# Performance work log

Hardware: AMD Instinct MI355X
Metric: run time of the kernel (lower is better)

Reference implementation:

```python
import jax, jax.numpy as jnp
import numpy as np

B, N = 128, 128
FEAT_IN = 6   # feature_dim(4) + class + score
E = 32        # embedding_dim
NUM_CLASSES = 80


def setup_inputs() -> dict:
    key = jax.random.key(0)
    ks = jax.random.split(key, 20)
    def glorot(k, shape):
        fan_in, fan_out = shape[0], shape[1]
        lim = jnp.sqrt(6.0 / (fan_in + fan_out)).astype(jnp.float32)
        return jax.random.uniform(k, shape, jnp.float32, -lim, lim)
    return {
        'boxes': jax.random.uniform(ks[0], (B, N, 4), jnp.float32),
        'classes': jax.random.randint(ks[1], (B, N), 0, NUM_CLASSES),
        'scores': jax.random.uniform(ks[2], (B, N), jnp.float32),
        'num_objects': jax.random.randint(ks[3], (B,), 1, N + 1),
        # feature_encoder: Linear(6->32), ReLU, Linear(32->32)
        'W1': glorot(ks[4], (FEAT_IN, E)), 'b1': jnp.zeros((E,), jnp.float32),
        'W2': glorot(ks[5], (E, E)),       'b2': jnp.zeros((E,), jnp.float32),
        # isObject: Linear(32->32), ReLU, Linear(32->1), Sigmoid
        'Wo1': glorot(ks[6], (E, E)),  'bo1': jnp.zeros((E,), jnp.float32),
        'Wo2': glorot(ks[7], (E, 1)),  'bo2': jnp.zeros((1,), jnp.float32),
        # sameClass: Linear(64->32), ReLU, Linear(32->1), Sigmoid
        'Ws1': glorot(ks[8], (2 * E, E)), 'bs1': jnp.zeros((E,), jnp.float32),
        'Ws2': glorot(ks[9], (E, 1)),     'bs2': jnp.zeros((1,), jnp.float32),
    }


def reference(boxes, classes, scores, num_objects, W1, b1, W2, b2,
              Wo1, bo1, Wo2, bo2, Ws1, bs1, Ws2, bs2):
    # encode: [B,N,6] -> [B,N,E]
    combined = jnp.concatenate(
        [boxes, classes.astype(jnp.float32)[..., None], scores[..., None]], axis=-1)
    enc = jax.nn.relu(combined @ W1 + b1) @ W2 + b2                 # [B,N,E]

    # isObject predicate -> [B,N]
    isobj = jax.nn.sigmoid(jax.nn.relu(enc @ Wo1 + bo1) @ Wo2 + bo2)[..., 0]

    # sameClass on all pairs: split concat-weight so we never build [B,N,N,2E]
    Wsx, Wsy = Ws1[:E], Ws1[E:]
    hx = enc @ Wsx                                                  # [B,N,E]
    hy = enc @ Wsy                                                  # [B,N,E]
    h = jax.nn.relu(hx[:, :, None, :] + hy[:, None, :, :] + bs1)    # [B,N,N,E]
    same = jax.nn.sigmoid(h @ Ws2 + bs2)[..., 0]                    # [B,N,N] (x,y)

    # inner = And_min(isObject(y), sameClass(x,y))
    inner = jnp.minimum(isobj[:, None, :], same)                    # [B,N,N]

    mask = jnp.arange(N)[None, :] < num_objects[:, None]            # [B,N] valid objs
    n = num_objects.astype(jnp.float32)
    denom = jnp.maximum(n, 1.0)

    # Exists_y = mean over valid y
    exists = jnp.sum(inner * mask[:, None, :], axis=-1) / denom[:, None]  # [B,N]

    # outer = Or_max(Not(isObject(x)), exists)
    outer = jnp.maximum(1.0 - isobj, exists)                        # [B,N]

    # Forall_x = min over valid x (pad with 1.0, never the min for valid batches)
    sat_b = jnp.min(jnp.where(mask, outer, 1.0), axis=-1)           # [B]

    valid = (num_objects > 0).astype(jnp.float32)
    cnt = jnp.sum(valid)
    total = jnp.where(cnt > 0,
                      jnp.sum(sat_b * valid) / jnp.maximum(cnt, 1.0),
                      jnp.float32(1.0))
    return total
```

## Files before the change

### kernel.cpp

```cpp
#include <hip/hip_runtime.h>

#define BB 128
#define NN 128
#define EE 32

#define SAT_OFF 0
#define CNT_OFF 128
#define HX_OFF  256
#define HY_OFF  (HX_OFF + 16384 * 32)
#define ISO_OFF (HY_OFF + 16384 * 32)

__global__ __launch_bounds__(256) void encode_kernel(
    const float* __restrict__ boxes, const int* __restrict__ classes,
    const float* __restrict__ scores,
    const float* __restrict__ W1, const float* __restrict__ b1,
    const float* __restrict__ W2, const float* __restrict__ b2,
    const float* __restrict__ Wo1, const float* __restrict__ bo1,
    const float* __restrict__ Wo2, const float* __restrict__ bo2,
    const float* __restrict__ Ws1, float* __restrict__ ws)
{
    __shared__ float rows[8 * 36];

    const int t = threadIdx.x;
    const int e = t & 31;
    const int g = t >> 5;

    if (blockIdx.x == 0) {
        if (t < 128) ((unsigned*)ws)[SAT_OFF + t] = 0x7F7F7F7Fu;
        if (t == 128) ((unsigned*)ws)[CNT_OFF] = 0u;
    }

    float w1c[6];
#pragma unroll
    for (int f = 0; f < 6; f++) w1c[f] = W1[f * 32 + e];
    float w2c[32], wo1c[32], wsxc[32], wsyc[32];
#pragma unroll
    for (int k = 0; k < 32; k++) {
        w2c[k]  = W2[k * 32 + e];
        wo1c[k] = Wo1[k * 32 + e];
        wsxc[k] = Ws1[k * 32 + e];
        wsyc[k] = Ws1[(32 + k) * 32 + e];
    }
    const float b1e  = b1[e];
    const float b2e  = b2[e];
    const float bo1e = bo1[e];
    const float wo2e = Wo2[e];
    const float bo2s = bo2[0];

    float* row = rows + g * 36;
    const int itemBase = blockIdx.x * 32 + g * 4;

#pragma unroll 1
    for (int it = 0; it < 4; ++it) {
        const int item = itemBase + it;

        const float4 bx = ((const float4*)boxes)[item];
        const float c4 = (float)classes[item];
        const float c5 = scores[item];

        float h1 = b1e;
        h1 = fmaf(bx.x, w1c[0], h1);
        h1 = fmaf(bx.y, w1c[1], h1);
        h1 = fmaf(bx.z, w1c[2], h1);
        h1 = fmaf(bx.w, w1c[3], h1);
        h1 = fmaf(c4,   w1c[4], h1);
        h1 = fmaf(c5,   w1c[5], h1);
        h1 = fmaxf(h1, 0.f);

        row[e] = h1;

        float a0 = 0.f, a1 = 0.f, a2 = 0.f, a3 = 0.f;
#pragma unroll
        for (int kk = 0; kk < 8; kk++) {
            const float4 h = *(const float4*)(row + kk * 4);
            a0 = fmaf(h.x, w2c[4 * kk + 0], a0);
            a1 = fmaf(h.y, w2c[4 * kk + 1], a1);
            a2 = fmaf(h.z, w2c[4 * kk + 2], a2);
            a3 = fmaf(h.w, w2c[4 * kk + 3], a3);
        }
        const float enc = ((a0 + a1) + (a2 + a3)) + b2e;
        row[e] = enc;

        float u = bo1e, hx = 0.f, hy = 0.f;
#pragma unroll
        for (int kk = 0; kk < 8; kk++) {
            const float4 ec = *(const float4*)(row + kk * 4);
            const int k0 = 4 * kk;
            u  = fmaf(ec.x, wo1c[k0 + 0], u);
            u  = fmaf(ec.y, wo1c[k0 + 1], u);
            u  = fmaf(ec.z, wo1c[k0 + 2], u);
            u  = fmaf(ec.w, wo1c[k0 + 3], u);
            hx = fmaf(ec.x, wsxc[k0 + 0], hx);
            hx = fmaf(ec.y, wsxc[k0 + 1], hx);
            hx = fmaf(ec.z, wsxc[k0 + 2], hx);
            hx = fmaf(ec.w, wsxc[k0 + 3], hx);
            hy = fmaf(ec.x, wsyc[k0 + 0], hy);
            hy = fmaf(ec.y, wsyc[k0 + 1], hy);
            hy = fmaf(ec.z, wsyc[k0 + 2], hy);
            hy = fmaf(ec.w, wsyc[k0 + 3], hy);
        }
        u = fmaxf(u, 0.f);

        float v = u * wo2e;
        v += __shfl_xor(v, 16, 32);
        v += __shfl_xor(v, 8, 32);
        v += __shfl_xor(v, 4, 32);
        v += __shfl_xor(v, 2, 32);
        v += __shfl_xor(v, 1, 32);

        ws[HX_OFF + item * 32 + e] = hx;
        ws[HY_OFF + item * 32 + e] = hy;
        if (e == 0)
            ws[ISO_OFF + item] = 1.f / (1.f + __expf(-(v + bo2s)));
    }
}

__global__ __launch_bounds__(256) void pairs_kernel(
    const float* __restrict__ bs1, const float* __restrict__ Ws2,
    const float* __restrict__ bs2, const int* __restrict__ num_objects,
    float* __restrict__ ws, float* __restrict__ out, int nblocks)
{
    __shared__ float hyS[128 * 36];
    __shared__ float hxS[64 * 36];
    __shared__ float isoS[128];
    __shared__ float wred[4];
    __shared__ int lastFlag;
    __shared__ float r1[4], r2[4];

    const int t = threadIdx.x;
    const int b = blockIdx.x >> 1;
    const int half = blockIdx.x & 1;

    const float4* hyg4 = (const float4*)(ws + HY_OFF + b * 128 * 32);
#pragma unroll
    for (int it = 0; it < 4; it++) {
        const int idx = t + it * 256;
        ((float4*)(hyS + (idx >> 3) * 36))[idx & 7] = hyg4[idx];
    }
    const float4* hxg4 = (const float4*)(ws + HX_OFF + (b * 128 + half * 64) * 32);
#pragma unroll
    for (int it = 0; it < 2; it++) {
        const int idx = t + it * 256;
        ((float4*)(hxS + (idx >> 3) * 36))[idx & 7] = hxg4[idx];
    }
    if (t < 128) isoS[t] = ws[ISO_OFF + b * 128 + t];
    __syncthreads();

    const int nb = num_objects[b];
    const int p  = t >> 3;
    const int i0 = half * 64 + p * 2;
    const int i1 = i0 + 1;
    const int s  = t & 7;

    float hxb0[32], hxb1[32];
#pragma unroll
    for (int kk = 0; kk < 8; kk++) {
        const float4 a = ((const float4*)(hxS + (p * 2) * 36))[kk];
        const float4 c = ((const float4*)(hxS + (p * 2 + 1) * 36))[kk];
        const int k0 = 4 * kk;
        hxb0[k0 + 0] = a.x + bs1[k0 + 0];  hxb1[k0 + 0] = c.x + bs1[k0 + 0];
        hxb0[k0 + 1] = a.y + bs1[k0 + 1];  hxb1[k0 + 1] = c.y + bs1[k0 + 1];
        hxb0[k0 + 2] = a.z + bs1[k0 + 2];  hxb1[k0 + 2] = c.z + bs1[k0 + 2];
        hxb0[k0 + 3] = a.w + bs1[k0 + 3];  hxb1[k0 + 3] = c.w + bs1[k0 + 3];
    }
    float w2[32];
#pragma unroll
    for (int k = 0; k < 32; k++) w2[k] = Ws2[k];
    const float bbias = bs2[0];

    float acc0 = 0.f, acc1 = 0.f;
    for (int j = s; j < nb; j += 8) {
        const float4* hr4 = (const float4*)(hyS + j * 36);
        float d0 = bbias, d1 = 0.f, d2 = 0.f, d3 = 0.f;
        float e0 = bbias, e1 = 0.f, e2 = 0.f, e3 = 0.f;
#pragma unroll
        for (int kk = 0; kk < 8; kk++) {
            const float4 h = hr4[kk];
            const int k0 = 4 * kk;
            d0 = fmaf(fmaxf(hxb0[k0 + 0] + h.x, 0.f), w2[k0 + 0], d0);
            d1 = fmaf(fmaxf(hxb0[k0 + 1] + h.y, 0.f), w2[k0 + 1], d1);
            d2 = fmaf(fmaxf(hxb0[k0 + 2] + h.z, 0.f), w2[k0 + 2], d2);
            d3 = fmaf(fmaxf(hxb0[k0 + 3] + h.w, 0.f), w2[k0 + 3], d3);
            e0 = fmaf(fmaxf(hxb1[k0 + 0] + h.x, 0.f), w2[k0 + 0], e0);
            e1 = fmaf(fmaxf(hxb1[k0 + 1] + h.y, 0.f), w2[k0 + 1], e1);
            e2 = fmaf(fmaxf(hxb1[k0 + 2] + h.z, 0.f), w2[k0 + 2], e2);
            e3 = fmaf(fmaxf(hxb1[k0 + 3] + h.w, 0.f), w2[k0 + 3], e3);
        }
        const float dd = (d0 + d1) + (d2 + d3);
        const float ee = (e0 + e1) + (e2 + e3);
        const float same0 = 1.f / (1.f + __expf(-dd));
        const float same1 = 1.f / (1.f + __expf(-ee));
        const float iso_j = isoS[j];
        acc0 += fminf(iso_j, same0);
        acc1 += fminf(iso_j, same1);
    }
    acc0 += __shfl_xor(acc0, 1);  acc1 += __shfl_xor(acc1, 1);
    acc0 += __shfl_xor(acc0, 2);  acc1 += __shfl_xor(acc1, 2);
    acc0 += __shfl_xor(acc0, 4);  acc1 += __shfl_xor(acc1, 4);

    const float denom = (float)(nb > 1 ? nb : 1);
    const float ex0 = acc0 / denom;
    const float ex1 = acc1 / denom;
    const float o0 = fmaxf(1.f - isoS[i0], ex0);
    const float o1 = fmaxf(1.f - isoS[i1], ex1);
    float val = fminf((i0 < nb) ? o0 : 1.f, (i1 < nb) ? o1 : 1.f);

    val = fminf(val, __shfl_xor(val, 8));
    val = fminf(val, __shfl_xor(val, 16));
    val = fminf(val, __shfl_xor(val, 32));
    if ((t & 63) == 0) wred[t >> 6] = val;
    __syncthreads();

    if (t == 0) {
        const float m = fminf(fminf(wred[0], wred[1]), fminf(wred[2], wred[3]));
        atomicMin((unsigned*)ws + SAT_OFF + b, __float_as_uint(m));
        __threadfence();
        const unsigned old = __hip_atomic_fetch_add((unsigned*)ws + CNT_OFF, 1u,
                                                    __ATOMIC_ACQ_REL, __HIP_MEMORY_SCOPE_AGENT);
        lastFlag = (old == (unsigned)(nblocks - 1)) ? 1 : 0;
    }
    __syncthreads();

    if (lastFlag) {
        float contrib = 0.f, vcnt = 0.f;
        if (t < 128) {
            const int nbt = num_objects[t];
            const unsigned sbits = __hip_atomic_load((unsigned*)ws + SAT_OFF + t,
                                                     __ATOMIC_RELAXED, __HIP_MEMORY_SCOPE_AGENT);
            const float sat = __uint_as_float(sbits);
            const float valid = (nbt > 0) ? 1.f : 0.f;
            contrib = sat * valid;
            vcnt = valid;
        }
#pragma unroll
        for (int off = 1; off < 64; off <<= 1) {
            contrib += __shfl_xor(contrib, off);
            vcnt += __shfl_xor(vcnt, off);
        }
        if ((t & 63) == 0) { r1[t >> 6] = contrib; r2[t >> 6] = vcnt; }
        __syncthreads();
        if (t == 0) {
            const float sc = r1[0] + r1[1] + r1[2] + r1[3];
            const float cn = r2[0] + r2[1] + r2[2] + r2[3];
            out[0] = (cn > 0.f) ? (sc / cn) : 1.f;
        }
    }
}

extern "C" void kernel_launch(void* const* d_in, const int* in_sizes, int n_in,
                              void* d_out, int out_size, void* d_ws, size_t ws_size,
                              hipStream_t stream)
{
    const float* boxes       = (const float*)d_in[0];
    const int*   classes     = (const int*)d_in[1];
    const float* scores      = (const float*)d_in[2];
    const int*   num_objects = (const int*)d_in[3];
    const float* W1  = (const float*)d_in[4];
    const float* b1  = (const float*)d_in[5];
    const float* W2  = (const float*)d_in[6];
    const float* b2  = (const float*)d_in[7];
    const float* Wo1 = (const float*)d_in[8];
    const float* bo1 = (const float*)d_in[9];
    const float* Wo2 = (const float*)d_in[10];
    const float* bo2 = (const float*)d_in[11];
    const float* Ws1 = (const float*)d_in[12];
    const float* bs1 = (const float*)d_in[13];
    const float* Ws2 = (const float*)d_in[14];
    const float* bs2 = (const float*)d_in[15];

    float* ws  = (float*)d_ws;
    float* out = (float*)d_out;

    encode_kernel<<<512, 256, 0, stream>>>(boxes, classes, scores,
                                           W1, b1, W2, b2, Wo1, bo1, Wo2, bo2,
                                           Ws1, ws);
    const int nblocks = 128 * 2;
    pairs_kernel<<<nblocks, 256, 0, stream>>>(bs1, Ws2, bs2, num_objects,
                                              ws, out, nblocks);
}
```

Baseline: 102.4 us.

## Fuse encoder into pair kernel and replace atomic last-block reduction with finalize kernel

Merges the per-object encoder into the pair kernel. Each block recomputes the encodings for all 128 objects of its batch and keeps hx, hy and isObject in shared memory instead of writing them to global workspace and reading them back. The atomicMin/counter last-block reduction becomes per-block partial minima plus a tiny one-block finalize kernel. This removes the global round trip and the atomics, but every batch's encoding is now computed twice (once per half-block), and the 256-block fused kernel carries more shared memory and serial per-thread encode work (16 items per warp).

Result: no change. 104.4 us (+1.9%).

```diff
diff --git a/kernel.cpp b/kernel.cpp
--- a/kernel.cpp
+++ b/kernel.cpp
@@ -4,31 +4,29 @@
 #define NN 128
 #define EE 32
 
-#define SAT_OFF 0
-#define CNT_OFF 128
-#define HX_OFF  256
-#define HY_OFF  (HX_OFF + 16384 * 32)
-#define ISO_OFF (HY_OFF + 16384 * 32)
-
-__global__ __launch_bounds__(256) void encode_kernel(
+
+__global__ __launch_bounds__(256) void ltn_fused(
     const float* __restrict__ boxes, const int* __restrict__ classes,
-    const float* __restrict__ scores,
+    const float* __restrict__ scores, const int* __restrict__ num_objects,
     const float* __restrict__ W1, const float* __restrict__ b1,
     const float* __restrict__ W2, const float* __restrict__ b2,
     const float* __restrict__ Wo1, const float* __restrict__ bo1,
     const float* __restrict__ Wo2, const float* __restrict__ bo2,
-    const float* __restrict__ Ws1, float* __restrict__ ws)
+    const float* __restrict__ Ws1, const float* __restrict__ bs1,
+    const float* __restrict__ Ws2, const float* __restrict__ bs2,
+    float* __restrict__ ws)
 {
-    __shared__ float rows[8 * 36];
+    __shared__ float hyS[128 * 36];
+    __shared__ float hxS[128 * 36];
+    __shared__ float rows[16 * 36];
+    __shared__ float isoS[128];
+    __shared__ float wred[4];
 
     const int t = threadIdx.x;
+    const int b = blockIdx.x >> 1;
+    const int half = blockIdx.x & 1;
     const int e = t & 31;
     const int g = t >> 5;
-
-    if (blockIdx.x == 0) {
-        if (t < 128) ((unsigned*)ws)[SAT_OFF + t] = 0x7F7F7F7Fu;
-        if (t == 128) ((unsigned*)ws)[CNT_OFF] = 0u;
-    }
 
     float w1c[6];
 #pragma unroll
@@ -47,12 +45,12 @@
     const float wo2e = Wo2[e];
     const float bo2s = bo2[0];
 
-    float* row = rows + g * 36;
-    const int itemBase = blockIdx.x * 32 + g * 4;
-
-#pragma unroll 1
-    for (int it = 0; it < 4; ++it) {
-        const int item = itemBase + it;
+    const int il0 = g * 16;
+#pragma unroll 2
+    for (int it = 0; it < 16; ++it) {
+        const int il = il0 + it;
+        const int item = b * 128 + il;
+        float* row = rows + (g * 2 + (it & 1)) * 36;
 
         const float4 bx = ((const float4*)boxes)[item];
         const float c4 = (float)classes[item];
@@ -108,55 +106,24 @@
         v += __shfl_xor(v, 2, 32);
         v += __shfl_xor(v, 1, 32);
 
-        ws[HX_OFF + item * 32 + e] = hx;
-        ws[HY_OFF + item * 32 + e] = hy;
+        hyS[il * 36 + e] = hy;
+        hxS[il * 36 + e] = hx;
         if (e == 0)
-            ws[ISO_OFF + item] = 1.f / (1.f + __expf(-(v + bo2s)));
-    }
-}
-
-__global__ __launch_bounds__(256) void pairs_kernel(
-    const float* __restrict__ bs1, const float* __restrict__ Ws2,
-    const float* __restrict__ bs2, const int* __restrict__ num_objects,
-    float* __restrict__ ws, float* __restrict__ out, int nblocks)
-{
-    __shared__ float hyS[128 * 36];
-    __shared__ float hxS[64 * 36];
-    __shared__ float isoS[128];
-    __shared__ float wred[4];
-    __shared__ int lastFlag;
-    __shared__ float r1[4], r2[4];
-
-    const int t = threadIdx.x;
-    const int b = blockIdx.x >> 1;
-    const int half = blockIdx.x & 1;
-
-    const float4* hyg4 = (const float4*)(ws + HY_OFF + b * 128 * 32);
-#pragma unroll
-    for (int it = 0; it < 4; it++) {
-        const int idx = t + it * 256;
-        ((float4*)(hyS + (idx >> 3) * 36))[idx & 7] = hyg4[idx];
-    }
-    const float4* hxg4 = (const float4*)(ws + HX_OFF + (b * 128 + half * 64) * 32);
-#pragma unroll
-    for (int it = 0; it < 2; it++) {
-        const int idx = t + it * 256;
-        ((float4*)(hxS + (idx >> 3) * 36))[idx & 7] = hxg4[idx];
-    }
-    if (t < 128) isoS[t] = ws[ISO_OFF + b * 128 + t];
+            isoS[il] = 1.f / (1.f + __expf(-(v + bo2s)));
+    }
     __syncthreads();
 
     const int nb = num_objects[b];
     const int p  = t >> 3;
-    const int i0 = half * 64 + p * 2;
-    const int i1 = i0 + 1;
+    const int li0 = half * 64 + p * 2;
+    const int li1 = li0 + 1;
     const int s  = t & 7;
 
     float hxb0[32], hxb1[32];
 #pragma unroll
     for (int kk = 0; kk < 8; kk++) {
-        const float4 a = ((const float4*)(hxS + (p * 2) * 36))[kk];
-        const float4 c = ((const float4*)(hxS + (p * 2 + 1) * 36))[kk];
+        const float4 a = ((const float4*)(hxS + li0 * 36))[kk];
+        const float4 c = ((const float4*)(hxS + li1 * 36))[kk];
         const int k0 = 4 * kk;
         hxb0[k0 + 0] = a.x + bs1[k0 + 0];  hxb1[k0 + 0] = c.x + bs1[k0 + 0];
         hxb0[k0 + 1] = a.y + bs1[k0 + 1];  hxb1[k0 + 1] = c.y + bs1[k0 + 1];
@@ -201,9 +168,9 @@
     const float denom = (float)(nb > 1 ? nb : 1);
     const float ex0 = acc0 / denom;
     const float ex1 = acc1 / denom;
-    const float o0 = fmaxf(1.f - isoS[i0], ex0);
-    const float o1 = fmaxf(1.f - isoS[i1], ex1);
-    float val = fminf((i0 < nb) ? o0 : 1.f, (i1 < nb) ? o1 : 1.f);
+    const float o0 = fmaxf(1.f - isoS[li0], ex0);
+    const float o1 = fmaxf(1.f - isoS[li1], ex1);
+    float val = fminf((li0 < nb) ? o0 : 1.f, (li1 < nb) ? o1 : 1.f);
 
     val = fminf(val, __shfl_xor(val, 8));
     val = fminf(val, __shfl_xor(val, 16));
@@ -211,39 +178,31 @@
     if ((t & 63) == 0) wred[t >> 6] = val;
     __syncthreads();
 
+    if (t == 0)
+        ws[blockIdx.x] = fminf(fminf(wred[0], wred[1]), fminf(wred[2], wred[3]));
+}
+
+__global__ __launch_bounds__(128) void finalize_kernel(
+    const int* __restrict__ num_objects, const float* __restrict__ ws,
+    float* __restrict__ out)
+{
+    __shared__ float r1[2], r2[2];
+    const int t = threadIdx.x;
+    const float sat = fminf(ws[2 * t], ws[2 * t + 1]);
+    const float valid = (num_objects[t] > 0) ? 1.f : 0.f;
+    float contrib = sat * valid;
+    float vcnt = valid;
+#pragma unroll
+    for (int off = 1; off < 64; off <<= 1) {
+        contrib += __shfl_xor(contrib, off);
+        vcnt    += __shfl_xor(vcnt, off);
+    }
+    if ((t & 63) == 0) { r1[t >> 6] = contrib; r2[t >> 6] = vcnt; }
+    __syncthreads();
     if (t == 0) {
-        const float m = fminf(fminf(wred[0], wred[1]), fminf(wred[2], wred[3]));
-        atomicMin((unsigned*)ws + SAT_OFF + b, __float_as_uint(m));
-        __threadfence();
-        const unsigned old = __hip_atomic_fetch_add((unsigned*)ws + CNT_OFF, 1u,
-                                                    __ATOMIC_ACQ_REL, __HIP_MEMORY_SCOPE_AGENT);
-        lastFlag = (old == (unsigned)(nblocks - 1)) ? 1 : 0;
-    }
-    __syncthreads();
-
-    if (lastFlag) {
-        float contrib = 0.f, vcnt = 0.f;
-        if (t < 128) {
-            const int nbt = num_objects[t];
-            const unsigned sbits = __hip_atomic_load((unsigned*)ws + SAT_OFF + t,
-                                                     __ATOMIC_RELAXED, __HIP_MEMORY_SCOPE_AGENT);
-            const float sat = __uint_as_float(sbits);
-            const float valid = (nbt > 0) ? 1.f : 0.f;
-            contrib = sat * valid;
-            vcnt = valid;
-        }
-#pragma unroll
-        for (int off = 1; off < 64; off <<= 1) {
-            contrib += __shfl_xor(contrib, off);
-            vcnt += __shfl_xor(vcnt, off);
-        }
-        if ((t & 63) == 0) { r1[t >> 6] = contrib; r2[t >> 6] = vcnt; }
-        __syncthreads();
-        if (t == 0) {
-            const float sc = r1[0] + r1[1] + r1[2] + r1[3];
-            const float cn = r2[0] + r2[1] + r2[2] + r2[3];
-            out[0] = (cn > 0.f) ? (sc / cn) : 1.f;
-        }
+        const float sc = r1[0] + r1[1];
+        const float cn = r2[0] + r2[1];
+        out[0] = (cn > 0.f) ? (sc / cn) : 1.f;
     }
 }
 
@@ -271,10 +230,8 @@
     float* ws  = (float*)d_ws;
     float* out = (float*)d_out;
 
-    encode_kernel<<<512, 256, 0, stream>>>(boxes, classes, scores,
-                                           W1, b1, W2, b2, Wo1, bo1, Wo2, bo2,
-                                           Ws1, ws);
-    const int nblocks = 128 * 2;
-    pairs_kernel<<<nblocks, 256, 0, stream>>>(bs1, Ws2, bs2, num_objects,
-                                              ws, out, nblocks);
+    ltn_fused<<<256, 256, 0, stream>>>(boxes, classes, scores, num_objects,
+                                       W1, b1, W2, b2, Wo1, bo1, Wo2, bo2,
+                                       Ws1, bs1, Ws2, bs2, ws);
+    finalize_kernel<<<1, 128, 0, stream>>>(num_objects, ws, out);
 }
```
